# Kernel optimization log

Measured on AMD Instinct MI355X. Metric: run time of the kernel, lower is better.

Reference implementation:

```python
import jax, jax.numpy as jnp
import numpy as np

N_NODES = 50000


def gcn_conv(x, W, b, src, dst, n):
    """PyG GCNConv: add self-loops, sym-normalize, linear, scatter-add."""
    loop = jnp.arange(n, dtype=src.dtype)
    s = jnp.concatenate([src, loop])  # [E+N]
    d = jnp.concatenate([dst, loop])
    deg = jax.ops.segment_sum(jnp.ones_like(s, dtype=x.dtype), d, num_segments=n)
    dinv = jnp.where(deg > 0, jax.lax.rsqrt(deg), 0.0)  # deg^-1/2
    norm = dinv[s] * dinv[d]  # [E+N]
    h = x @ W  # [N, out] dense GEMM first (in >= out)
    msg = h[s] * norm[:, None]  # gather + scale
    out = jax.ops.segment_sum(msg, d, num_segments=n)  # scatter-add
    return out + b


def setup_inputs() -> dict:
    key = jax.random.key(0)
    k1, k2, k3, k4, k5, k6, k7, k8 = jax.random.split(key, 8)
    in_c, hid_c, out_c = 512, 128, 64
    n, e, l = N_NODES, 800000, 100000
    x = jax.random.normal(k1, (n, in_c), dtype=jnp.float32)
    edge_index = jax.random.randint(k2, (2, e), 0, n, dtype=jnp.int64)
    edge_label_index = jax.random.randint(k3, (2, l), 0, n, dtype=jnp.int64)
    # Glorot-ish init for weights, zeros for biases (PyG default bias=zeros)
    W1 = jax.random.normal(k4, (in_c, hid_c), dtype=jnp.float32) / np.sqrt(in_c)
    b1 = jnp.zeros((hid_c,), dtype=jnp.float32)
    W2 = jax.random.normal(k5, (hid_c, out_c), dtype=jnp.float32) / np.sqrt(hid_c)
    b2 = jnp.zeros((out_c,), dtype=jnp.float32)
    return {"x": x, "edge_index": edge_index, "edge_label_index": edge_label_index,
            "W1": W1, "b1": b1, "W2": W2, "b2": b2}


def reference(x, edge_index, edge_label_index, W1, b1, W2, b2):
    n = x.shape[0]
    src, dst = edge_index[0], edge_index[1]
    z = jax.nn.relu(gcn_conv(x, W1, b1, src, dst, n))
    z = gcn_conv(z, W2, b2, src, dst, n)
    es, ed = edge_label_index[0], edge_label_index[1]
    return jnp.sum(z[es] * z[ed], axis=-1).reshape(-1)
```

## Files before the change

### kernel.cpp

```cpp
#include <hip/hip_runtime.h>

#define IN_C  512
#define HID_C 128
#define OUT_C 64

using short8 = __attribute__((ext_vector_type(8))) short;
using floatx4 = __attribute__((ext_vector_type(4))) float;

__device__ inline unsigned short f2bf(float f) {
    unsigned u = __builtin_bit_cast(unsigned, f);
    u += 0x7FFFu + ((u >> 16) & 1u);
    return (unsigned short)(u >> 16);
}
__device__ inline float bf2f(unsigned short h) {
    unsigned u = ((unsigned)h) << 16;
    return __builtin_bit_cast(float, u);
}
__device__ inline unsigned short f2h(float f) {
    _Float16 h = (_Float16)f;
    return __builtin_bit_cast(unsigned short, h);
}
__device__ inline float h2f(unsigned v) {
    return (float)__builtin_bit_cast(_Float16, (unsigned short)v);
}

__global__ void k_zero_int(int* __restrict__ p, int n) {
    int i = blockIdx.x * blockDim.x + threadIdx.x;
    if (i < n) p[i] = 0;
}

__global__ void k_count(const int* __restrict__ dst, int* __restrict__ cnt, int e) {
    int i = blockIdx.x * blockDim.x + threadIdx.x;
    if (i < e) atomicAdd(&cnt[dst[i]], 1);
}

__global__ void k_dinv(const int* __restrict__ cnt, float* __restrict__ dinv, int n) {
    int i = blockIdx.x * blockDim.x + threadIdx.x;
    if (i < n) dinv[i] = rsqrtf(1.0f + (float)cnt[i]);
}

__global__ void k_blocksum(const int* __restrict__ cnt, int* __restrict__ bsum, int n) {
    __shared__ int sdata[256];
    int t = threadIdx.x;
    int i = blockIdx.x * 256 + t;
    sdata[t] = (i < n) ? cnt[i] : 0;
    __syncthreads();
    for (int s = 128; s > 0; s >>= 1) {
        if (t < s) sdata[t] += sdata[t + s];
        __syncthreads();
    }
    if (t == 0) bsum[blockIdx.x] = sdata[0];
}

__global__ void k_scanpartials(int* __restrict__ bsum, int nb) {
    __shared__ int sdata[256];
    int t = threadIdx.x;
    int orig = (t < nb) ? bsum[t] : 0;
    sdata[t] = orig;
    __syncthreads();
    for (int off = 1; off < 256; off <<= 1) {
        int v = (t >= off) ? sdata[t - off] : 0;
        __syncthreads();
        sdata[t] += v;
        __syncthreads();
    }
    if (t < nb) bsum[t] = sdata[t] - orig;
}

__global__ void k_scanfinal(const int* __restrict__ cnt, const int* __restrict__ bsum_ex,
                            int* __restrict__ row_ptr, int n, int e_total) {
    __shared__ int sdata[256];
    int t = threadIdx.x;
    int i = blockIdx.x * 256 + t;
    int orig = (i < n) ? cnt[i] : 0;
    sdata[t] = orig;
    __syncthreads();
    for (int off = 1; off < 256; off <<= 1) {
        int v = (t >= off) ? sdata[t - off] : 0;
        __syncthreads();
        sdata[t] += v;
        __syncthreads();
    }
    if (i < n) row_ptr[i] = sdata[t] - orig + bsum_ex[blockIdx.x];
    if (i == 0) row_ptr[n] = e_total;
}

__global__ void k_fill(const int* __restrict__ src, const int* __restrict__ dst,
                       const int* __restrict__ row_ptr, int* __restrict__ cur,
                       int* __restrict__ col, int e) {
    int i = blockIdx.x * blockDim.x + threadIdx.x;
    if (i < e) {
        int d = dst[i];
        int pos = atomicAdd(&cur[d], 1);
        col[row_ptr[d] + pos] = src[i];
    }
}

__global__ void k_prep_w(const float* __restrict__ W, unsigned short* __restrict__ hi,
                         unsigned short* __restrict__ lo, int K, int N) {
    int i = blockIdx.x * blockDim.x + threadIdx.x;
    if (i >= K * N) return;
    int k = i / N, n = i % N;
    float v = W[i];
    unsigned short h = f2bf(v);
    float r = v - bf2f(h);
    hi[(long)n * K + k] = h;
    lo[(long)n * K + k] = f2bf(r);
}

template <int K, int NPW>
__global__ __launch_bounds__(256) void k_gemm_mfma(
    const float* __restrict__ A, const unsigned short* __restrict__ Bt_hi,
    const unsigned short* __restrict__ Bt_lo, const float* __restrict__ dinv,
    unsigned short* __restrict__ Hs, int M) {
    constexpr int N = 64 * NPW;
    constexpr int LDA = 72;
    constexpr int NT = K / 64;
    __shared__ __align__(16) unsigned short As_hi[2][64 * LDA];
    __shared__ __align__(16) unsigned short As_lo[2][64 * LDA];

    const int tid = threadIdx.x;
    const int w = tid >> 6;
    const int lane = tid & 63;
    const int m = lane & 15;
    const int quad = lane >> 4;
    const int m0 = blockIdx.x * 64;

    const int srow = tid >> 4;
    const int skk = (tid & 15) << 2;

    floatx4 acc[4][NPW];
#pragma unroll
    for (int mi = 0; mi < 4; ++mi)
#pragma unroll
        for (int ni = 0; ni < NPW; ++ni) acc[mi][ni] = (floatx4){0.f, 0.f, 0.f, 0.f};

    float4 pf[4];
#pragma unroll
    for (int i = 0; i < 4; ++i) {
        int gm = m0 + srow + 16 * i;
        pf[i] = make_float4(0.f, 0.f, 0.f, 0.f);
        if (gm < M) pf[i] = *(const float4*)&A[(long)gm * K + skk];
    }
#pragma unroll
    for (int i = 0; i < 4; ++i) {
        ushort4 h, l;
        h.x = f2bf(pf[i].x); l.x = f2bf(pf[i].x - bf2f(h.x));
        h.y = f2bf(pf[i].y); l.y = f2bf(pf[i].y - bf2f(h.y));
        h.z = f2bf(pf[i].z); l.z = f2bf(pf[i].z - bf2f(h.z));
        h.w = f2bf(pf[i].w); l.w = f2bf(pf[i].w - bf2f(h.w));
        int off = (srow + 16 * i) * LDA + skk;
        *(ushort4*)&As_hi[0][off] = h;
        *(ushort4*)&As_lo[0][off] = l;
    }

    for (int t = 0; t < NT; ++t) {
        __syncthreads();
        const int buf = t & 1;
        if (t + 1 < NT) {
#pragma unroll
            for (int i = 0; i < 4; ++i) {
                int gm = m0 + srow + 16 * i;
                pf[i] = make_float4(0.f, 0.f, 0.f, 0.f);
                if (gm < M) pf[i] = *(const float4*)&A[(long)gm * K + (t + 1) * 64 + skk];
            }
        }
#pragma unroll
        for (int s = 0; s < 2; ++s) {
            short8 ah[4], al[4];
#pragma unroll
            for (int mi = 0; mi < 4; ++mi) {
                int off = (mi * 16 + m) * LDA + s * 32 + quad * 8;
                ah[mi] = *(const short8*)&As_hi[buf][off];
                al[mi] = *(const short8*)&As_lo[buf][off];
            }
#pragma unroll
            for (int ni = 0; ni < NPW; ++ni) {
                int n = (w * NPW + ni) * 16 + m;
                long boff = (long)n * K + t * 64 + s * 32 + quad * 8;
                short8 bh = *(const short8*)&Bt_hi[boff];
                short8 bl = *(const short8*)&Bt_lo[boff];
#pragma unroll
                for (int mi = 0; mi < 4; ++mi) {
                    acc[mi][ni] = __builtin_amdgcn_mfma_f32_16x16x32_bf16(ah[mi], bh, acc[mi][ni], 0, 0, 0);
                    acc[mi][ni] = __builtin_amdgcn_mfma_f32_16x16x32_bf16(ah[mi], bl, acc[mi][ni], 0, 0, 0);
                    acc[mi][ni] = __builtin_amdgcn_mfma_f32_16x16x32_bf16(al[mi], bh, acc[mi][ni], 0, 0, 0);
                }
            }
        }
        if (t + 1 < NT) {
#pragma unroll
            for (int i = 0; i < 4; ++i) {
                ushort4 h, l;
                h.x = f2bf(pf[i].x); l.x = f2bf(pf[i].x - bf2f(h.x));
                h.y = f2bf(pf[i].y); l.y = f2bf(pf[i].y - bf2f(h.y));
                h.z = f2bf(pf[i].z); l.z = f2bf(pf[i].z - bf2f(h.z));
                h.w = f2bf(pf[i].w); l.w = f2bf(pf[i].w - bf2f(h.w));
                int off = (srow + 16 * i) * LDA + skk;
                *(ushort4*)&As_hi[buf ^ 1][off] = h;
                *(ushort4*)&As_lo[buf ^ 1][off] = l;
            }
        }
    }

#pragma unroll
    for (int mi = 0; mi < 4; ++mi) {
#pragma unroll
        for (int r = 0; r < 4; ++r) {
            int row = m0 + mi * 16 + quad * 4 + r;
            if (row < M) {
                float dv = dinv[row];
#pragma unroll
                for (int ni = 0; ni < NPW; ++ni) {
                    int n = (w * NPW + ni) * 16 + m;
                    Hs[(long)row * N + n] = f2h(acc[mi][ni][r] * dv);
                }
            }
        }
    }
}

__global__ __launch_bounds__(256) void k_agg1(
    const unsigned short* __restrict__ h, const int* __restrict__ row_ptr,
    const int* __restrict__ col, const float* __restrict__ dinv,
    const float* __restrict__ bias, float* __restrict__ z, int n) {
    int node = blockIdx.x * 4 + (threadIdx.x >> 6);
    node = __builtin_amdgcn_readfirstlane(node);
    if (node >= n) return;
    int lane = threadIdx.x & 63;
    int half = lane >> 5, li = lane & 31;
    const uint2* hp = (const uint2*)h;
    float4 acc = make_float4(0.f, 0.f, 0.f, 0.f);
    if (half == 0) {
        uint2 v = hp[(long)node * 32 + li];
        acc.x = h2f(v.x); acc.y = h2f(v.x >> 16);
        acc.z = h2f(v.y); acc.w = h2f(v.y >> 16);
    }
    int rs = row_ptr[node], re = row_ptr[node + 1];
    int cnt = re - rs, pairs = cnt >> 1;
    int j = rs + half;
    int p = 0;
    for (; p + 4 <= pairs; p += 4, j += 8) {
        int s0 = col[j], s1 = col[j + 2], s2 = col[j + 4], s3 = col[j + 6];
        uint2 v0 = hp[(long)s0 * 32 + li];
        uint2 v1 = hp[(long)s1 * 32 + li];
        uint2 v2 = hp[(long)s2 * 32 + li];
        uint2 v3 = hp[(long)s3 * 32 + li];
        acc.x += h2f(v0.x) + h2f(v1.x) + h2f(v2.x) + h2f(v3.x);
        acc.y += h2f(v0.x >> 16) + h2f(v1.x >> 16) + h2f(v2.x >> 16) + h2f(v3.x >> 16);
        acc.z += h2f(v0.y) + h2f(v1.y) + h2f(v2.y) + h2f(v3.y);
        acc.w += h2f(v0.y >> 16) + h2f(v1.y >> 16) + h2f(v2.y >> 16) + h2f(v3.y >> 16);
    }
    for (; p < pairs; ++p, j += 2) {
        int s = col[j];
        uint2 v = hp[(long)s * 32 + li];
        acc.x += h2f(v.x); acc.y += h2f(v.x >> 16);
        acc.z += h2f(v.y); acc.w += h2f(v.y >> 16);
    }
    if ((cnt & 1) && half == 0) {
        int s = col[re - 1];
        uint2 v = hp[(long)s * 32 + li];
        acc.x += h2f(v.x); acc.y += h2f(v.x >> 16);
        acc.z += h2f(v.y); acc.w += h2f(v.y >> 16);
    }
    float ox = __shfl(acc.x, li + 32);
    float oy = __shfl(acc.y, li + 32);
    float oz = __shfl(acc.z, li + 32);
    float ow = __shfl(acc.w, li + 32);
    if (half == 0) {
        acc.x += ox; acc.y += oy; acc.z += oz; acc.w += ow;
        float dv = dinv[node];
        float4 b = ((const float4*)bias)[li];
        float4 o;
        o.x = fmaxf(fmaf(acc.x, dv, b.x), 0.f);
        o.y = fmaxf(fmaf(acc.y, dv, b.y), 0.f);
        o.z = fmaxf(fmaf(acc.z, dv, b.z), 0.f);
        o.w = fmaxf(fmaf(acc.w, dv, b.w), 0.f);
        ((float4*)z)[(long)node * 32 + li] = o;
    }
}

__global__ __launch_bounds__(256) void k_agg2(
    const unsigned short* __restrict__ h, const int* __restrict__ row_ptr,
    const int* __restrict__ col, const float* __restrict__ dinv,
    const float* __restrict__ bias, float* __restrict__ z, int n) {
    int node = blockIdx.x * 4 + (threadIdx.x >> 6);
    node = __builtin_amdgcn_readfirstlane(node);
    if (node >= n) return;
    int lane = threadIdx.x & 63;
    int half = lane >> 5, li = lane & 31;
    const unsigned* hp = (const unsigned*)h;
    float2 acc = make_float2(0.f, 0.f);
    if (half == 0) {
        unsigned v = hp[(long)node * 32 + li];
        acc.x = h2f(v); acc.y = h2f(v >> 16);
    }
    int rs = row_ptr[node], re = row_ptr[node + 1];
    int cnt = re - rs, pairs = cnt >> 1;
    int j = rs + half;
    int p = 0;
    for (; p + 4 <= pairs; p += 4, j += 8) {
        int s0 = col[j], s1 = col[j + 2], s2 = col[j + 4], s3 = col[j + 6];
        unsigned v0 = hp[(long)s0 * 32 + li];
        unsigned v1 = hp[(long)s1 * 32 + li];
        unsigned v2 = hp[(long)s2 * 32 + li];
        unsigned v3 = hp[(long)s3 * 32 + li];
        acc.x += h2f(v0) + h2f(v1) + h2f(v2) + h2f(v3);
        acc.y += h2f(v0 >> 16) + h2f(v1 >> 16) + h2f(v2 >> 16) + h2f(v3 >> 16);
    }
    for (; p < pairs; ++p, j += 2) {
        unsigned v = hp[(long)col[j] * 32 + li];
        acc.x += h2f(v); acc.y += h2f(v >> 16);
    }
    if ((cnt & 1) && half == 0) {
        unsigned v = hp[(long)col[re - 1] * 32 + li];
        acc.x += h2f(v); acc.y += h2f(v >> 16);
    }
    float ox = __shfl(acc.x, li + 32);
    float oy = __shfl(acc.y, li + 32);
    if (half == 0) {
        acc.x += ox; acc.y += oy;
        float dv = dinv[node];
        float2 b = ((const float2*)bias)[li];
        float2 o;
        o.x = fmaf(acc.x, dv, b.x);
        o.y = fmaf(acc.y, dv, b.y);
        ((float2*)z)[(long)node * 32 + li] = o;
    }
}

__global__ void k_dot(const float* __restrict__ z2, const int* __restrict__ es,
                      const int* __restrict__ ed, float* __restrict__ out, int L) {
    int gid = blockIdx.x * blockDim.x + threadIdx.x;
    int wid = gid >> 6;
    int lane = threadIdx.x & 63;
    if (wid >= L) return;
    int a = es[wid], b = ed[wid];
    float v = z2[(long)a * OUT_C + lane] * z2[(long)b * OUT_C + lane];
#pragma unroll
    for (int off = 32; off > 0; off >>= 1) v += __shfl_down(v, off);
    if (lane == 0) out[wid] = v;
}

extern "C" void kernel_launch(void* const* d_in, const int* in_sizes, int n_in,
                              void* d_out, int out_size, void* d_ws, size_t ws_size,
                              hipStream_t stream) {
    const float* x = (const float*)d_in[0];
    const int* ei = (const int*)d_in[1];
    const int* eli = (const int*)d_in[2];
    const float* W1 = (const float*)d_in[3];
    const float* b1 = (const float*)d_in[4];
    const float* W2 = (const float*)d_in[5];
    const float* b2 = (const float*)d_in[6];
    float* out = (float*)d_out;

    const int N = in_sizes[0] / IN_C;
    const int E = in_sizes[1] / 2;
    const int L = in_sizes[2] / 2;
    const int* src = ei;
    const int* dst = ei + E;
    const int* es = eli;
    const int* ed = eli + L;

    const int Npad = (N + 63) & ~63;
    const int Epad = (E + 3) & ~3;

    int* cnt = (int*)d_ws;
    int* cur = cnt + Npad;
    int* row_ptr = cur + Npad;
    int* bsum = row_ptr + Npad + 64;
    int* col = bsum + 256;
    float* dinv = (float*)(col + Epad);
    unsigned short* h1s = (unsigned short*)(dinv + Npad);
    float* z1 = (float*)(h1s + (long)N * HID_C);
    unsigned short* h2s = h1s;
    float* z2 = z1 + (long)N * HID_C;
    unsigned short* wt1_hi = (unsigned short*)(z2 + (long)N * OUT_C);
    unsigned short* wt1_lo = wt1_hi + IN_C * HID_C;
    unsigned short* wt2_hi = wt1_lo + IN_C * HID_C;
    unsigned short* wt2_lo = wt2_hi + HID_C * OUT_C;

    const int TPB = 256;
    const int nb = (N + 255) / 256;

    k_prep_w<<<(IN_C * HID_C + TPB - 1) / TPB, TPB, 0, stream>>>(W1, wt1_hi, wt1_lo, IN_C, HID_C);
    k_prep_w<<<(HID_C * OUT_C + TPB - 1) / TPB, TPB, 0, stream>>>(W2, wt2_hi, wt2_lo, HID_C, OUT_C);

    k_zero_int<<<(2 * Npad + TPB - 1) / TPB, TPB, 0, stream>>>(cnt, 2 * Npad);
    k_count<<<(E + TPB - 1) / TPB, TPB, 0, stream>>>(dst, cnt, E);
    k_dinv<<<(N + TPB - 1) / TPB, TPB, 0, stream>>>(cnt, dinv, N);
    k_blocksum<<<nb, 256, 0, stream>>>(cnt, bsum, N);
    k_scanpartials<<<1, 256, 0, stream>>>(bsum, nb);
    k_scanfinal<<<nb, 256, 0, stream>>>(cnt, bsum, row_ptr, N, E);
    k_fill<<<(E + TPB - 1) / TPB, TPB, 0, stream>>>(src, dst, row_ptr, cur, col, E);

    k_gemm_mfma<IN_C, 2><<<(N + 63) / 64, 256, 0, stream>>>(x, wt1_hi, wt1_lo, dinv, h1s, N);
    k_agg1<<<(N + 3) / 4, 256, 0, stream>>>(h1s, row_ptr, col, dinv, b1, z1, N);

    k_gemm_mfma<HID_C, 1><<<(N + 63) / 64, 256, 0, stream>>>(z1, wt2_hi, wt2_lo, dinv, h2s, N);
    k_agg2<<<(N + 3) / 4, 256, 0, stream>>>(h2s, row_ptr, col, dinv, b2, z2, N);

    k_dot<<<((long)L * 64 + TPB - 1) / TPB, TPB, 0, stream>>>(z2, es, ed, out, L);
}
```

Before: 380.1 us.

## Prefetch GEMM B fragments, fuse small prep kernels, halve dot-kernel waves

The MFMA GEMM main loop is unrolled by two, and the B (weight) fragments are loaded into registers one tile ahead so global latency overlaps compute. Several launches are merged: dinv is folded into the block-sum kernel and both weight preps share one kernel. The fill step reuses the count array through atomicSub, which drops a separate cursor array and half of the zeroing. The link-dot kernel now handles two edges per wave using float2 loads. The cost is higher register pressure in the GEMM from the extra prefetch buffers.

```diff
diff --git a/kernel.cpp b/kernel.cpp
--- a/kernel.cpp
+++ b/kernel.cpp
@@ -34,16 +34,14 @@
     if (i < e) atomicAdd(&cnt[dst[i]], 1);
 }
 
-__global__ void k_dinv(const int* __restrict__ cnt, float* __restrict__ dinv, int n) {
-    int i = blockIdx.x * blockDim.x + threadIdx.x;
-    if (i < n) dinv[i] = rsqrtf(1.0f + (float)cnt[i]);
-}
-
-__global__ void k_blocksum(const int* __restrict__ cnt, int* __restrict__ bsum, int n) {
+__global__ void k_blocksum_dinv(const int* __restrict__ cnt, int* __restrict__ bsum,
+                                float* __restrict__ dinv, int n) {
     __shared__ int sdata[256];
     int t = threadIdx.x;
     int i = blockIdx.x * 256 + t;
-    sdata[t] = (i < n) ? cnt[i] : 0;
+    int c = (i < n) ? cnt[i] : 0;
+    if (i < n) dinv[i] = rsqrtf(1.0f + (float)c);
+    sdata[t] = c;
     __syncthreads();
     for (int s = 128; s > 0; s >>= 1) {
         if (t < s) sdata[t] += sdata[t + s];
@@ -86,26 +84,34 @@
 }
 
 __global__ void k_fill(const int* __restrict__ src, const int* __restrict__ dst,
-                       const int* __restrict__ row_ptr, int* __restrict__ cur,
+                       const int* __restrict__ row_ptr, int* __restrict__ cnt,
                        int* __restrict__ col, int e) {
     int i = blockIdx.x * blockDim.x + threadIdx.x;
     if (i < e) {
         int d = dst[i];
-        int pos = atomicAdd(&cur[d], 1);
+        int pos = atomicSub(&cnt[d], 1) - 1;
         col[row_ptr[d] + pos] = src[i];
     }
 }
 
-__global__ void k_prep_w(const float* __restrict__ W, unsigned short* __restrict__ hi,
-                         unsigned short* __restrict__ lo, int K, int N) {
+__global__ void k_prep_w2(const float* __restrict__ W1, unsigned short* __restrict__ hi1,
+                          unsigned short* __restrict__ lo1, const float* __restrict__ W2,
+                          unsigned short* __restrict__ hi2, unsigned short* __restrict__ lo2) {
     int i = blockIdx.x * blockDim.x + threadIdx.x;
-    if (i >= K * N) return;
-    int k = i / N, n = i % N;
-    float v = W[i];
-    unsigned short h = f2bf(v);
-    float r = v - bf2f(h);
-    hi[(long)n * K + k] = h;
-    lo[(long)n * K + k] = f2bf(r);
+    if (i < IN_C * HID_C) {
+        int k = i / HID_C, n = i % HID_C;
+        float v = W1[i];
+        unsigned short h = f2bf(v);
+        hi1[(long)n * IN_C + k] = h;
+        lo1[(long)n * IN_C + k] = f2bf(v - bf2f(h));
+    } else if (i < IN_C * HID_C + HID_C * OUT_C) {
+        int j = i - IN_C * HID_C;
+        int k = j / OUT_C, n = j % OUT_C;
+        float v = W2[j];
+        unsigned short h = f2bf(v);
+        hi2[(long)n * HID_C + k] = h;
+        lo2[(long)n * HID_C + k] = f2bf(v - bf2f(h));
+    }
 }
 
 template <int K, int NPW>
@@ -116,6 +122,7 @@
     constexpr int N = 64 * NPW;
     constexpr int LDA = 72;
     constexpr int NT = K / 64;
+    static_assert((NT & 1) == 0, "NT must be even");
     __shared__ __align__(16) unsigned short As_hi[2][64 * LDA];
     __shared__ __align__(16) unsigned short As_lo[2][64 * LDA];
 
@@ -136,71 +143,80 @@
         for (int ni = 0; ni < NPW; ++ni) acc[mi][ni] = (floatx4){0.f, 0.f, 0.f, 0.f};
 
     float4 pf[4];
-#pragma unroll
-    for (int i = 0; i < 4; ++i) {
-        int gm = m0 + srow + 16 * i;
-        pf[i] = make_float4(0.f, 0.f, 0.f, 0.f);
-        if (gm < M) pf[i] = *(const float4*)&A[(long)gm * K + skk];
-    }
-#pragma unroll
-    for (int i = 0; i < 4; ++i) {
-        ushort4 h, l;
-        h.x = f2bf(pf[i].x); l.x = f2bf(pf[i].x - bf2f(h.x));
-        h.y = f2bf(pf[i].y); l.y = f2bf(pf[i].y - bf2f(h.y));
-        h.z = f2bf(pf[i].z); l.z = f2bf(pf[i].z - bf2f(h.z));
-        h.w = f2bf(pf[i].w); l.w = f2bf(pf[i].w - bf2f(h.w));
-        int off = (srow + 16 * i) * LDA + skk;
-        *(ushort4*)&As_hi[0][off] = h;
-        *(ushort4*)&As_lo[0][off] = l;
-    }
-
-    for (int t = 0; t < NT; ++t) {
-        __syncthreads();
-        const int buf = t & 1;
-        if (t + 1 < NT) {
-#pragma unroll
-            for (int i = 0; i < 4; ++i) {
-                int gm = m0 + srow + 16 * i;
-                pf[i] = make_float4(0.f, 0.f, 0.f, 0.f);
-                if (gm < M) pf[i] = *(const float4*)&A[(long)gm * K + (t + 1) * 64 + skk];
+    short8 b0h[2][NPW], b0l[2][NPW], b1h[2][NPW], b1l[2][NPW];
+
+    auto issueA = [&](int t0) {
+#pragma unroll
+        for (int i = 0; i < 4; ++i) {
+            int gm = m0 + srow + 16 * i;
+            pf[i] = make_float4(0.f, 0.f, 0.f, 0.f);
+            if (gm < M) pf[i] = *(const float4*)&A[(long)gm * K + t0 * 64 + skk];
+        }
+    };
+    auto convA = [&](int b) {
+#pragma unroll
+        for (int i = 0; i < 4; ++i) {
+            ushort4 h, l;
+            h.x = f2bf(pf[i].x); l.x = f2bf(pf[i].x - bf2f(h.x));
+            h.y = f2bf(pf[i].y); l.y = f2bf(pf[i].y - bf2f(h.y));
+            h.z = f2bf(pf[i].z); l.z = f2bf(pf[i].z - bf2f(h.z));
+            h.w = f2bf(pf[i].w); l.w = f2bf(pf[i].w - bf2f(h.w));
+            int off = (srow + 16 * i) * LDA + skk;
+            *(ushort4*)&As_hi[b][off] = h;
+            *(ushort4*)&As_lo[b][off] = l;
+        }
+    };
+    auto loadB = [&](short8 bh[2][NPW], short8 bl[2][NPW], int t0) {
+        if (t0 >= NT) return;
+#pragma unroll
+        for (int s = 0; s < 2; ++s)
+#pragma unroll
+            for (int ni = 0; ni < NPW; ++ni) {
+                int n = (w * NPW + ni) * 16 + m;
+                long boff = (long)n * K + t0 * 64 + s * 32 + quad * 8;
+                bh[s][ni] = *(const short8*)&Bt_hi[boff];
+                bl[s][ni] = *(const short8*)&Bt_lo[boff];
             }
-        }
+    };
+    auto compute = [&](int b, short8 bh[2][NPW], short8 bl[2][NPW]) {
 #pragma unroll
         for (int s = 0; s < 2; ++s) {
             short8 ah[4], al[4];
 #pragma unroll
             for (int mi = 0; mi < 4; ++mi) {
                 int off = (mi * 16 + m) * LDA + s * 32 + quad * 8;
-                ah[mi] = *(const short8*)&As_hi[buf][off];
-                al[mi] = *(const short8*)&As_lo[buf][off];
+                ah[mi] = *(const short8*)&As_hi[b][off];
+                al[mi] = *(const short8*)&As_lo[b][off];
             }
 #pragma unroll
             for (int ni = 0; ni < NPW; ++ni) {
-                int n = (w * NPW + ni) * 16 + m;
-                long boff = (long)n * K + t * 64 + s * 32 + quad * 8;
-                short8 bh = *(const short8*)&Bt_hi[boff];
-                short8 bl = *(const short8*)&Bt_lo[boff];
 #pragma unroll
                 for (int mi = 0; mi < 4; ++mi) {
-                    acc[mi][ni] = __builtin_amdgcn_mfma_f32_16x16x32_bf16(ah[mi], bh, acc[mi][ni], 0, 0, 0);
-                    acc[mi][ni] = __builtin_amdgcn_mfma_f32_16x16x32_bf16(ah[mi], bl, acc[mi][ni], 0, 0, 0);
-                    acc[mi][ni] = __builtin_amdgcn_mfma_f32_16x16x32_bf16(al[mi], bh, acc[mi][ni], 0, 0, 0);
+                    acc[mi][ni] = __builtin_amdgcn_mfma_f32_16x16x32_bf16(ah[mi], bh[s][ni], acc[mi][ni], 0, 0, 0);
+                    acc[mi][ni] = __builtin_amdgcn_mfma_f32_16x16x32_bf16(ah[mi], bl[s][ni], acc[mi][ni], 0, 0, 0);
+                    acc[mi][ni] = __builtin_amdgcn_mfma_f32_16x16x32_bf16(al[mi], bh[s][ni], acc[mi][ni], 0, 0, 0);
                 }
             }
         }
-        if (t + 1 < NT) {
-#pragma unroll
-            for (int i = 0; i < 4; ++i) {
-                ushort4 h, l;
-                h.x = f2bf(pf[i].x); l.x = f2bf(pf[i].x - bf2f(h.x));
-                h.y = f2bf(pf[i].y); l.y = f2bf(pf[i].y - bf2f(h.y));
-                h.z = f2bf(pf[i].z); l.z = f2bf(pf[i].z - bf2f(h.z));
-                h.w = f2bf(pf[i].w); l.w = f2bf(pf[i].w - bf2f(h.w));
-                int off = (srow + 16 * i) * LDA + skk;
-                *(ushort4*)&As_hi[buf ^ 1][off] = h;
-                *(ushort4*)&As_lo[buf ^ 1][off] = l;
-            }
-        }
+    };
+
+    issueA(0);
+    loadB(b0h, b0l, 0);
+    loadB(b1h, b1l, 1);
+    convA(0);
+
+#pragma unroll
+    for (int t = 0; t < NT; t += 2) {
+        __syncthreads();
+        issueA(t + 1);
+        compute(0, b0h, b0l);
+        loadB(b0h, b0l, t + 2);
+        convA(1);
+        __syncthreads();
+        if (t + 2 < NT) issueA(t + 2);
+        compute(1, b1h, b1l);
+        loadB(b1h, b1l, t + 3);
+        if (t + 2 < NT) convA(0);
     }
 
 #pragma unroll
@@ -334,12 +350,17 @@
     int gid = blockIdx.x * blockDim.x + threadIdx.x;
     int wid = gid >> 6;
     int lane = threadIdx.x & 63;
-    if (wid >= L) return;
-    int a = es[wid], b = ed[wid];
-    float v = z2[(long)a * OUT_C + lane] * z2[(long)b * OUT_C + lane];
-#pragma unroll
-    for (int off = 32; off > 0; off >>= 1) v += __shfl_down(v, off);
-    if (lane == 0) out[wid] = v;
+    int half = lane >> 5, li = lane & 31;
+    int e = wid * 2 + half;
+    if (e >= L) return;
+    int a = es[e], b = ed[e];
+    const float2* zp = (const float2*)z2;
+    float2 za = zp[(long)a * 32 + li];
+    float2 zb = zp[(long)b * 32 + li];
+    float v = za.x * zb.x + za.y * zb.y;
+#pragma unroll
+    for (int off = 16; off > 0; off >>= 1) v += __shfl_down(v, off);
+    if (li == 0) out[e] = v;
 }
 
 extern "C" void kernel_launch(void* const* d_in, const int* in_sizes, int n_in,
@@ -366,8 +387,7 @@
     const int Epad = (E + 3) & ~3;
 
     int* cnt = (int*)d_ws;
-    int* cur = cnt + Npad;
-    int* row_ptr = cur + Npad;
+    int* row_ptr = cnt + Npad;
     int* bsum = row_ptr + Npad + 64;
     int* col = bsum + 256;
     float* dinv = (float*)(col + Epad);
@@ -383,16 +403,15 @@
     const int TPB = 256;
     const int nb = (N + 255) / 256;
 
-    k_prep_w<<<(IN_C * HID_C + TPB - 1) / TPB, TPB, 0, stream>>>(W1, wt1_hi, wt1_lo, IN_C, HID_C);
-    k_prep_w<<<(HID_C * OUT_C + TPB - 1) / TPB, TPB, 0, stream>>>(W2, wt2_hi, wt2_lo, HID_C, OUT_C);
-
-    k_zero_int<<<(2 * Npad + TPB - 1) / TPB, TPB, 0, stream>>>(cnt, 2 * Npad);
+    const int PW = IN_C * HID_C + HID_C * OUT_C;
+    k_prep_w2<<<(PW + TPB - 1) / TPB, TPB, 0, stream>>>(W1, wt1_hi, wt1_lo, W2, wt2_hi, wt2_lo);
+
+    k_zero_int<<<(Npad + TPB - 1) / TPB, TPB, 0, stream>>>(cnt, Npad);
     k_count<<<(E + TPB - 1) / TPB, TPB, 0, stream>>>(dst, cnt, E);
-    k_dinv<<<(N + TPB - 1) / TPB, TPB, 0, stream>>>(cnt, dinv, N);
-    k_blocksum<<<nb, 256, 0, stream>>>(cnt, bsum, N);
+    k_blocksum_dinv<<<nb, 256, 0, stream>>>(cnt, bsum, dinv, N);
     k_scanpartials<<<1, 256, 0, stream>>>(bsum, nb);
     k_scanfinal<<<nb, 256, 0, stream>>>(cnt, bsum, row_ptr, N, E);
-    k_fill<<<(E + TPB - 1) / TPB, TPB, 0, stream>>>(src, dst, row_ptr, cur, col, E);
+    k_fill<<<(E + TPB - 1) / TPB, TPB, 0, stream>>>(src, dst, row_ptr, cnt, col, E);
 
     k_gemm_mfma<IN_C, 2><<<(N + 63) / 64, 256, 0, stream>>>(x, wt1_hi, wt1_lo, dinv, h1s, N);
     k_agg1<<<(N + 3) / 4, 256, 0, stream>>>(h1s, row_ptr, col, dinv, b1, z1, N);
@@ -400,5 +419,5 @@
     k_gemm_mfma<HID_C, 1><<<(N + 63) / 64, 256, 0, stream>>>(z1, wt2_hi, wt2_lo, dinv, h2s, N);
     k_agg2<<<(N + 3) / 4, 256, 0, stream>>>(h2s, row_ptr, col, dinv, b2, z2, N);
 
-    k_dot<<<((long)L * 64 + TPB - 1) / TPB, TPB, 0, stream>>>(z2, es, ed, out, L);
-}
+    k_dot<<<((long)((L + 1) / 2) * 64 + TPB - 1) / TPB, TPB, 0, stream>>>(z2, es, ed, out, L);
+}
```

After: 383.2 us. About the same (+0.8%).
